# Performance work log

Hardware: AMD Instinct MI355X
Metric: run time of the kernel (lower is better)

The kernel has to match this reference:

```python
import jax, jax.numpy as jnp
import numpy as np

N_X = 64          # grid points per side
DT = 1e-4         # time step
ALPHA = 1.0       # diffusivity
BATCH = 256


def _build_mats():
    """Dense Crank-Nicolson matrices A1 (implicit) and A0 (explicit) for the
    5-point heat stencil on an n_x * n_x grid, exactly as in the torch module."""
    n_x = N_X
    dx = 1.0 / n_x
    r = ALPHA * DT / dx / dx
    node = n_x * n_x
    d1 = np.ones((node,)) * (-2 * r + 1)
    d2 = np.ones((node,)) * (2 * r + 1)
    d3 = np.ones((node - 1,)) * (r / 2)
    d4 = np.ones((node - n_x,)) * (r / 2)
    A1 = (np.diag(d2) - np.diag(d3, -1) - np.diag(d3, 1)
          - np.diag(d4, -n_x) - np.diag(d4, n_x))
    A0 = (np.diag(d1) + np.diag(d3, -1) + np.diag(d3, 1)
          + np.diag(d4, -n_x) + np.diag(d4, n_x))
    return jnp.asarray(A1, jnp.float32), jnp.asarray(A0, jnp.float32)


def _boundary_mask():
    m = jnp.zeros((N_X, N_X), dtype=bool)
    m = m.at[0, :].set(True).at[-1, :].set(True)
    m = m.at[:, 0].set(True).at[:, -1].set(True)
    return m


def setup_inputs() -> dict:
    key = jax.random.key(0)
    A1, A0 = _build_mats()
    inp = jax.random.normal(key, (BATCH, N_X, N_X, 3), dtype=jnp.float32)
    return {"input": inp, "A1": A1, "A0": A0}


def reference(input, A1, A0):
    batch = input.shape[0]
    node = N_X * N_X
    # split channels: u(t), f(t), f(t+dt)
    x1 = input[..., 0].reshape(batch, node)   # (B, node)
    f0 = input[..., 1].reshape(batch, node)
    f1 = input[..., 2].reshape(batch, node)
    # rhs b = A0 @ x1 + dt * (f0 + f1)/2
    b = jnp.einsum('ij,bj->bi', A0, x1) + 0.5 * (f0 + f1) * DT  # (B, node)
    # one LU factorization of A1, multi-RHS solve across the batch
    sol = jnp.linalg.solve(A1, b.T).T.reshape(batch, N_X, N_X)
    # Dirichlet boundary: zero the border
    return jnp.where(_boundary_mask(), jnp.float32(0.0), sol)
```

## Files before the change

### kernel.cpp

```cpp
#include <hip/hip_runtime.h>


#define NX    64
#define NODE  (NX * NX)
#define NBATCH 256
#define HALO  64
#define LDSN  (NODE + 2 * HALO)
#define NITER 16
#define NT    512
#define NPT   (NODE / NT)

__global__ __launch_bounds__(NT, 1)
void heat_cn_kernel(const float* __restrict__ in, float* __restrict__ out) {
    __shared__ float xs[LDSN];
    __shared__ float u0[LDSN];
    __shared__ float u1[LDSN];

    const int t = threadIdx.x;
    const int batch = blockIdx.x;

    const float r    = 0.4096f;
    const float r2   = 0.2048f;
    const float d0   = 1.0f - 2.0f * r;
    const float invd = 1.0f / (1.0f + 2.0f * r);
    const float cc   = invd * r2;
    const float hdt  = 0.5f * 1e-4f;

    const float* __restrict__ src = in + (size_t)batch * NODE * 3;

    if (t < HALO) {
        xs[t] = 0.0f; xs[HALO + NODE + t] = 0.0f;
        u0[t] = 0.0f; u0[HALO + NODE + t] = 0.0f;
        u1[t] = 0.0f; u1[HALO + NODE + t] = 0.0f;
    }

    float fpart[NPT];
#pragma unroll
    for (int k = 0; k < NPT; ++k) {
        const int node = k * NT + t;
        const float x1 = src[node * 3 + 0];
        const float f0 = src[node * 3 + 1];
        const float f1 = src[node * 3 + 2];
        xs[HALO + node] = x1;
        fpart[k] = hdt * (f0 + f1);
    }
    __syncthreads();

    float bsc[NPT];
#pragma unroll
    for (int k = 0; k < NPT; ++k) {
        const int p = HALO + k * NT + t;
        const float nb = xs[p - 1] + xs[p + 1] + xs[p - 64] + xs[p + 64];
        const float bv = d0 * xs[p] + r2 * nb + fpart[k];
        bsc[k] = invd * bv;
        u0[p] = invd * bv;
    }
    __syncthreads();

#define JSTEP(UC, UN)                                                   \
    {                                                                   \
        _Pragma("unroll")                                               \
        for (int k = 0; k < NPT; ++k) {                                 \
            const int p = HALO + k * NT + t;                            \
            const float nb = UC[p - 1] + UC[p + 1] +                    \
                             UC[p - 64] + UC[p + 64];                   \
            UN[p] = fmaf(cc, nb, bsc[k]);                               \
        }                                                               \
        __syncthreads();                                                \
    }

    for (int it = 0; it < NITER / 2; ++it) {
        JSTEP(u0, u1)
        JSTEP(u1, u0)
    }
#undef JSTEP

    float* __restrict__ dst = out + (size_t)batch * NODE;
#pragma unroll
    for (int k = 0; k < NPT; ++k) {
        const int node = k * NT + t;
        const int i = node >> 6;
        const int j = node & 63;
        float v = u0[HALO + node];
        if (i == 0 || i == NX - 1 || j == 0 || j == NX - 1) v = 0.0f;
        dst[node] = v;
    }
}

extern "C" void kernel_launch(void* const* d_in, const int* in_sizes, int n_in,
                              void* d_out, int out_size, void* d_ws, size_t ws_size,
                              hipStream_t stream) {
    (void)in_sizes; (void)n_in; (void)d_ws; (void)ws_size; (void)out_size;
    const float* in = (const float*)d_in[0];
    float* out = (float*)d_out;
    heat_cn_kernel<<<NBATCH, NT, 0, stream>>>(in, out);
}
```

Measured before the change: 136.5 us.

## Replace Jacobi iterations with Chebyshev semi-iterative acceleration using fewer sweeps

Swaps the 16 plain Jacobi sweeps for one Jacobi step followed by 7 Chebyshev-accelerated steps with precomputed weights. The aim is to reach comparable solution accuracy with half the sweeps, cutting LDS traffic and barriers. It keeps two extra register arrays per thread and writes the final value from registers. Accuracy now depends on the spectral-radius estimate behind the weights.

Measured after the change: 132.3 us. -3.1%, faster.

```diff
diff --git a/kernel.cpp b/kernel.cpp
--- a/kernel.cpp
+++ b/kernel.cpp
@@ -6,9 +6,16 @@
 #define NBATCH 256
 #define HALO  64
 #define LDSN  (NODE + 2 * HALO)
-#define NITER 16
 #define NT    512
 #define NPT   (NODE / NT)
+
+#define W2 1.1128240f
+#define W3 1.0597800f
+#define W4 1.0567752f
+#define W5 1.0566050f
+#define W6 1.0565953f
+#define W7 1.0565948f
+#define W8 1.0565947f
 
 __global__ __launch_bounds__(NT, 1)
 void heat_cn_kernel(const float* __restrict__ in, float* __restrict__ out) {
@@ -47,33 +54,55 @@
     __syncthreads();
 
     float bsc[NPT];
+    float rcur[NPT];
+    float rprev[NPT];
 #pragma unroll
     for (int k = 0; k < NPT; ++k) {
         const int p = HALO + k * NT + t;
         const float nb = xs[p - 1] + xs[p + 1] + xs[p - 64] + xs[p + 64];
         const float bv = d0 * xs[p] + r2 * nb + fpart[k];
-        bsc[k] = invd * bv;
-        u0[p] = invd * bv;
+        const float g = invd * bv;
+        bsc[k] = g;
+        rcur[k] = g;
+        u0[p] = g;
     }
     __syncthreads();
 
-#define JSTEP(UC, UN)                                                   \
+#pragma unroll
+    for (int k = 0; k < NPT; ++k) {
+        const int p = HALO + k * NT + t;
+        const float nb = u0[p - 1] + u0[p + 1] + u0[p - 64] + u0[p + 64];
+        const float xn = fmaf(cc, nb, bsc[k]);
+        rprev[k] = rcur[k];
+        rcur[k] = xn;
+        u1[p] = xn;
+    }
+    __syncthreads();
+
+#define CHEB(UC, UN, W)                                                 \
     {                                                                   \
         _Pragma("unroll")                                               \
         for (int k = 0; k < NPT; ++k) {                                 \
             const int p = HALO + k * NT + t;                            \
             const float nb = UC[p - 1] + UC[p + 1] +                    \
                              UC[p - 64] + UC[p + 64];                   \
-            UN[p] = fmaf(cc, nb, bsc[k]);                               \
+            const float jac = fmaf(cc, nb, bsc[k]);                     \
+            const float xn = fmaf(W, jac - rprev[k], rprev[k]);         \
+            rprev[k] = rcur[k];                                         \
+            rcur[k] = xn;                                               \
+            UN[p] = xn;                                                 \
         }                                                               \
         __syncthreads();                                                \
     }
 
-    for (int it = 0; it < NITER / 2; ++it) {
-        JSTEP(u0, u1)
-        JSTEP(u1, u0)
-    }
-#undef JSTEP
+    CHEB(u1, u0, W2)
+    CHEB(u0, u1, W3)
+    CHEB(u1, u0, W4)
+    CHEB(u0, u1, W5)
+    CHEB(u1, u0, W6)
+    CHEB(u0, u1, W7)
+    CHEB(u1, u0, W8)
+#undef CHEB
 
     float* __restrict__ dst = out + (size_t)batch * NODE;
 #pragma unroll
@@ -81,7 +110,7 @@
         const int node = k * NT + t;
         const int i = node >> 6;
         const int j = node & 63;
-        float v = u0[HALO + node];
+        float v = rcur[k];
         if (i == 0 || i == NX - 1 || j == 0 || j == NX - 1) v = 0.0f;
         dst[node] = v;
     }
```
